# Kernel optimization log

Hardware: AMD Instinct MI355X
Metric: run time of the kernel (lower is better)

## Reference

```python
import jax, jax.numpy as jnp
import numpy as np

B, L, D, E = 16, 1024, 512, 8
DFF = 4 * D
N_VIEWS, N_BUCKETS = 4, 16


def setup_inputs() -> dict:
    key = jax.random.key(0)
    ks = jax.random.split(key, 9)
    s_in = 1.0 / np.sqrt(D)
    s_hid = 1.0 / np.sqrt(DFF)
    return {
        "x": jax.random.normal(ks[0], (B, L, D), dtype=jnp.float32),
        "view_ids": jax.random.randint(ks[1], (B,), 0, N_VIEWS),
        "visit_ids": jax.random.randint(ks[2], (B,), 0, N_BUCKETS),
        "router_view": jax.random.normal(ks[3], (N_VIEWS, E), dtype=jnp.float32),
        "router_visit": jax.random.normal(ks[4], (N_BUCKETS, E), dtype=jnp.float32),
        "W1": jax.random.uniform(ks[5], (E, D, DFF), jnp.float32, -s_in, s_in),
        "b1": jax.random.uniform(ks[6], (E, DFF), jnp.float32, -s_in, s_in),
        "W2": jax.random.uniform(ks[7], (E, DFF, D), jnp.float32, -s_hid, s_hid),
        "b2": jax.random.uniform(ks[8], (E, D), jnp.float32, -s_hid, s_hid),
    }


def reference(x, view_ids, visit_ids, router_view, router_visit, W1, b1, W2, b2):
    # Router: per-sample logits over experts, (B, E)
    logits = router_view[view_ids] + router_visit[visit_ids]
    top1 = jnp.argmax(logits, axis=-1)  # (B,)

    # Train-mode balance loss: load = mean softmax prob per expert, entropy-style term
    probs = jax.nn.softmax(logits, axis=-1)
    load = probs.mean(axis=0)  # (E,)
    balance_loss = -jnp.sum(load * jnp.log(load))

    # Per-sample expert FFN: gather each sample's expert weights (dense grouped GEMM
    # equivalent of the original masked gather->FFN->scatter loop).
    w1 = W1[top1]                      # (B, D, DFF)
    w2 = W2[top1]                      # (B, DFF, D)
    h = jax.nn.relu(jnp.einsum("bld,bdf->blf", x, w1) + b1[top1][:, None, :])
    out = jnp.einsum("blf,bfd->bld", h, w2) + b2[top1][:, None, :]
    return out, balance_loss
```

## Files before the change

### kernel.cpp

```cpp
#include <hip/hip_runtime.h>
#include <stdint.h>

#define B_SZ 16
#define L_SZ 1024
#define D_SZ 512
#define E_SZ 8
#define DFF_SZ 2048

typedef short bf16x8 __attribute__((ext_vector_type(8)));
typedef float f32x4 __attribute__((ext_vector_type(4)));

__device__ __forceinline__ unsigned short f2bf(float f) {
  unsigned int u = __float_as_uint(f);
  u += 0x7fffu + ((u >> 16) & 1u);
  return (unsigned short)(u >> 16);
}

__device__ __forceinline__ void async_cp16(void* lds, const void* g) {
  __builtin_amdgcn_global_load_lds(
      (const __attribute__((address_space(1))) void*)g,
      (__attribute__((address_space(3))) void*)lds, 16, 0, 0);
}

__global__ void router_kernel(const int* __restrict__ view_ids,
                              const int* __restrict__ visit_ids,
                              const float* __restrict__ rview,
                              const float* __restrict__ rvisit,
                              int* __restrict__ top1,
                              float* __restrict__ loss_out) {
  __shared__ float probs[B_SZ][E_SZ];
  const int t = threadIdx.x;
  if (t < B_SZ) {
    const int vi = view_ids[t];
    const int si = visit_ids[t];
    float lg[E_SZ];
#pragma unroll
    for (int e = 0; e < E_SZ; ++e)
      lg[e] = rview[vi * E_SZ + e] + rvisit[si * E_SZ + e];
    int am = 0;
    float bm = lg[0];
#pragma unroll
    for (int e = 1; e < E_SZ; ++e)
      if (lg[e] > bm) { bm = lg[e]; am = e; }
    top1[t] = am;
    float s = 0.f;
#pragma unroll
    for (int e = 0; e < E_SZ; ++e) {
      const float p = expf(lg[e] - bm);
      probs[t][e] = p;
      s += p;
    }
    const float inv = 1.f / s;
#pragma unroll
    for (int e = 0; e < E_SZ; ++e) probs[t][e] *= inv;
  }
  __syncthreads();
  if (t == 0) {
    float loss = 0.f;
#pragma unroll
    for (int e = 0; e < E_SZ; ++e) {
      float ld = 0.f;
      for (int b = 0; b < B_SZ; ++b) ld += probs[b][e];
      ld *= (1.0f / B_SZ);
      loss -= ld * logf(ld);
    }
    *loss_out = loss;
  }
}

__global__ void cast_x_kernel(const float* __restrict__ x,
                              unsigned short* __restrict__ xb) {
  const int i = blockIdx.x * 256 + threadIdx.x;
  const float4 v = reinterpret_cast<const float4*>(x)[i];
  ushort4 o;
  o.x = f2bf(v.x); o.y = f2bf(v.y); o.z = f2bf(v.z); o.w = f2bf(v.w);
  reinterpret_cast<ushort4*>(xb)[i] = o;
}

__global__ void transpose_cast_kernel(const float* __restrict__ src,
                                      unsigned short* __restrict__ dst,
                                      int K, int N) {
  __shared__ float tile[64][65];
  const int e = blockIdx.z;
  const int n0 = blockIdx.x * 64;
  const int k0 = blockIdx.y * 64;
  const int t = threadIdx.x;
  const int c = t & 63;
  const int r4 = t >> 6;
  const float* s = src + ((size_t)e * K + k0) * N + n0;
#pragma unroll
  for (int it = 0; it < 16; ++it) {
    const int k = it * 4 + r4;
    tile[k][c] = s[(size_t)k * N + c];
  }
  __syncthreads();
  unsigned short* d = dst + ((size_t)e * N + n0) * K + k0;
#pragma unroll
  for (int it = 0; it < 16; ++it) {
    const int n = it * 4 + r4;
    d[(size_t)n * K + c] = f2bf(tile[c][n]);
  }
}

template <int BN, int WN2, int NTILES, bool RELU, bool OUT_BF16>
__global__ __launch_bounds__(512, 2) void gemm8_kernel(
    const unsigned short* __restrict__ A,
    const unsigned short* __restrict__ BT,
    const float* __restrict__ bias,
    const int* __restrict__ top1,
    void* __restrict__ Out,
    int N, int K) {
  constexpr int HB = BN / 2;
  constexpr int WM2 = 8 / WN2;
  constexpr int RPA = 128 / WM2;
  constexpr int RPB = HB / WN2;
  constexpr int MF = RPA / 16;
  constexpr int NF = RPB / 16;
  constexpr int LB = HB / 64;
  constexpr int ABUF = 2 * 128 * 64;
  constexpr int BBUF = 2 * HB * 64;
  constexpr int BUFSZ = ABUF + BBUF;

  __shared__ __align__(16) unsigned short sm[2 * BUFSZ];

  const int t = threadIdx.x;
  const int lane = t & 63;
  const int wid = t >> 6;
  const int wm2 = wid / WN2;
  const int wn2 = wid % WN2;
  const int lr = lane & 15, lg = lane >> 4;

  const int nwg = gridDim.x;
  const int bid = blockIdx.x;
  const int wg = (bid & 7) * (nwg >> 3) + (bid >> 3);
  const int mt = wg / NTILES;
  const int nt = wg % NTILES;
  const int n0 = nt * BN;
  const int bz = mt >> 2;
  const int e = top1[bz];

  const size_t Kb = (size_t)K * 2;
  const int srow = t >> 3;
  const int sgr = (t & 7) ^ (srow & 7);
  const char* aRow = (const char*)A + ((size_t)mt * 256 + srow) * Kb + sgr * 16;
  const char* bRow =
      (const char*)BT + ((size_t)e * N + n0 + srow) * Kb + sgr * 16;

  auto stageA = [&](int buf, int half, int kt) {
    char* dst = (char*)sm + (size_t)(buf * BUFSZ + half * (128 * 64)) * 2 + t * 16;
    const char* s = aRow + (size_t)(half * 128) * Kb + (size_t)kt * 128;
    async_cp16(dst, s);
    async_cp16(dst + 8192, s + 64 * Kb);
  };
  auto stageB = [&](int buf, int half, int kt) {
    char* dst =
        (char*)sm + (size_t)(buf * BUFSZ + ABUF + half * (HB * 64)) * 2 + t * 16;
    const char* s = bRow + (size_t)(half * HB) * Kb + (size_t)kt * 128;
    async_cp16(dst, s);
    if constexpr (LB == 2) async_cp16(dst + 8192, s + 64 * Kb);
  };

  f32x4 acc[2][2][MF][NF] = {};
  const int nk = K >> 6;

  stageA(0, 0, 0); stageB(0, 0, 0); stageA(0, 1, 0); stageB(0, 1, 0);
  stageA(1, 0, 1); stageB(1, 0, 1);
  if constexpr (LB == 2) asm volatile("s_waitcnt vmcnt(4)" ::: "memory");
  else                   asm volatile("s_waitcnt vmcnt(3)" ::: "memory");
  __builtin_amdgcn_s_barrier();
  asm volatile("" ::: "memory");

#define PHASE(QM, QN, STAGE_STMT, TAIL_STMT)                                   \
  {                                                                            \
    const char* ab =                                                           \
        (const char*)sm + (size_t)(bi * BUFSZ + (QM) * (128 * 64)) * 2;        \
    const char* bbp =                                                          \
        (const char*)sm + (size_t)(bi * BUFSZ + ABUF + (QN) * (HB * 64)) * 2;  \
    bf16x8 af[MF][2], bg[NF][2];                                               \
    _Pragma("unroll") for (int mf = 0; mf < MF; ++mf) {                        \
      const int row = wm2 * RPA + mf * 16 + lr;                                \
      _Pragma("unroll") for (int ks = 0; ks < 2; ++ks)                         \
          af[mf][ks] = *(const bf16x8*)(ab + row * 128 +                       \
                                        (((ks * 4 + lg) ^ (lr & 7)) << 4));    \
    }                                                                          \
    _Pragma("unroll") for (int nf = 0; nf < NF; ++nf) {                        \
      const int row = wn2 * RPB + nf * 16 + lr;                                \
      _Pragma("unroll") for (int ks = 0; ks < 2; ++ks)                         \
          bg[nf][ks] = *(const bf16x8*)(bbp + row * 128 +                      \
                                        (((ks * 4 + lg) ^ (lr & 7)) << 4));    \
    }                                                                          \
    STAGE_STMT                                                                 \
    __builtin_amdgcn_s_barrier();                                              \
    asm volatile("" ::: "memory");                                             \
    __builtin_amdgcn_s_setprio(1);                                             \
    _Pragma("unroll") for (int ks = 0; ks < 2; ++ks)                           \
        _Pragma("unroll") for (int mf = 0; mf < MF; ++mf)                      \
            _Pragma("unroll") for (int nf = 0; nf < NF; ++nf)                  \
                acc[QM][QN][mf][nf] = __builtin_amdgcn_mfma_f32_16x16x32_bf16( \
                    af[mf][ks], bg[nf][ks], acc[QM][QN][mf][nf], 0, 0, 0);     \
    __builtin_amdgcn_s_setprio(0);                                             \
    TAIL_STMT                                                                  \
    __builtin_amdgcn_s_barrier();                                              \
    asm volatile("" ::: "memory");                                             \
  }

  for (int kt = 0; kt < nk; ++kt) {
    const int bi = kt & 1;
    PHASE(0, 0, { if (kt + 1 < nk) stageA(bi ^ 1, 1, kt + 1); }, {})
    PHASE(0, 1, { if (kt + 1 < nk) stageB(bi ^ 1, 1, kt + 1); }, {})
    PHASE(1, 0, { if (kt + 2 < nk) stageA(bi, 0, kt + 2); }, {})
    PHASE(1, 1, { if (kt + 2 < nk) stageB(bi, 0, kt + 2); },
          {
            if (kt + 2 < nk) {
              if constexpr (LB == 2)
                asm volatile("s_waitcnt vmcnt(4)" ::: "memory");
              else
                asm volatile("s_waitcnt vmcnt(3)" ::: "memory");
            } else {
              asm volatile("s_waitcnt vmcnt(0)" ::: "memory");
            }
          })
  }
#undef PHASE

  const size_t mrow0 = (size_t)mt * 256;
  const float* bp = bias + (size_t)e * N + n0;
  unsigned short* ho = (unsigned short*)Out;
  float* fo = (float*)Out;
#pragma unroll
  for (int qm = 0; qm < 2; ++qm)
#pragma unroll
    for (int mf = 0; mf < MF; ++mf) {
      const int row0 = qm * 128 + wm2 * RPA + mf * 16 + lg * 4;
#pragma unroll
      for (int qn = 0; qn < 2; ++qn)
#pragma unroll
        for (int nf = 0; nf < NF; ++nf) {
          const int col = qn * HB + wn2 * RPB + nf * 16 + lr;
          const float bv = bp[col];
#pragma unroll
          for (int r = 0; r < 4; ++r) {
            float v = acc[qm][qn][mf][nf][r] + bv;
            if (RELU) v = fmaxf(v, 0.f);
            const size_t o = (mrow0 + row0 + r) * (size_t)N + n0 + col;
            if (OUT_BF16) ho[o] = f2bf(v);
            else fo[o] = v;
          }
        }
    }
}

extern "C" void kernel_launch(void* const* d_in, const int* in_sizes, int n_in,
                              void* d_out, int out_size, void* d_ws,
                              size_t ws_size, hipStream_t stream) {
  const float* x = (const float*)d_in[0];
  const int* view_ids = (const int*)d_in[1];
  const int* visit_ids = (const int*)d_in[2];
  const float* rview = (const float*)d_in[3];
  const float* rvisit = (const float*)d_in[4];
  const float* W1 = (const float*)d_in[5];
  const float* b1 = (const float*)d_in[6];
  const float* W2 = (const float*)d_in[7];
  const float* b2 = (const float*)d_in[8];
  float* out = (float*)d_out;

  char* ws = (char*)d_ws;
  int* top1 = (int*)ws;
  unsigned short* x_bf = (unsigned short*)(ws + 256);
  unsigned short* w1t = (unsigned short*)(ws + 256 + 16777216L);
  unsigned short* w2t = (unsigned short*)(ws + 256 + 2 * 16777216L);
  unsigned short* h_bf = (unsigned short*)(ws + 256 + 3 * 16777216L);

  router_kernel<<<1, 64, 0, stream>>>(view_ids, visit_ids, rview, rvisit, top1,
                                      out + (size_t)B_SZ * L_SZ * D_SZ);
  cast_x_kernel<<<8192, 256, 0, stream>>>(x, x_bf);
  transpose_cast_kernel<<<dim3(DFF_SZ / 64, D_SZ / 64, E_SZ), 256, 0, stream>>>(
      W1, w1t, D_SZ, DFF_SZ);
  transpose_cast_kernel<<<dim3(D_SZ / 64, DFF_SZ / 64, E_SZ), 256, 0, stream>>>(
      W2, w2t, DFF_SZ, D_SZ);

  gemm8_kernel<256, 4, 8, true, true><<<512, 512, 0, stream>>>(
      x_bf, w1t, b1, top1, (void*)h_bf, DFF_SZ, D_SZ);
  gemm8_kernel<128, 2, 4, false, false><<<256, 512, 0, stream>>>(
      h_bf, w2t, b2, top1, (void*)out, D_SZ, DFF_SZ);
}
```

Before: 255.1 us.

## Reuse A/B LDS fragments across quadrant phases and vectorize weight transpose-cast

The GEMM main loop now keeps A fragments in registers across the two N-quadrants and keeps both B fragment halves, so each K-step reads A and B from LDS once per half instead of once per quadrant. This cuts LDS read traffic and ds_read instructions in the MFMA loop, at the cost of more live VGPRs (two B fragment sets), which may pressure the 512-thread, 2-waves launch bound. The transpose-cast kernel also switches to float4 global loads and ushort4 stores to reduce memory instruction count.

Measured after the change: 245.3 us. -3.9%, faster.

```diff
diff --git a/kernel.cpp b/kernel.cpp
--- a/kernel.cpp
+++ b/kernel.cpp
@@ -85,20 +85,31 @@
   const int n0 = blockIdx.x * 64;
   const int k0 = blockIdx.y * 64;
   const int t = threadIdx.x;
-  const int c = t & 63;
-  const int r4 = t >> 6;
-  const float* s = src + ((size_t)e * K + k0) * N + n0;
-#pragma unroll
-  for (int it = 0; it < 16; ++it) {
-    const int k = it * 4 + r4;
-    tile[k][c] = s[(size_t)k * N + c];
+  {
+    const int c4 = (t & 15) * 4;
+    const int r = t >> 4;
+    const float* s = src + ((size_t)e * K + k0) * N + n0;
+#pragma unroll
+    for (int i = 0; i < 4; ++i) {
+      const int k = r + i * 16;
+      const float4 v = *(const float4*)(s + (size_t)k * N + c4);
+      tile[k][c4] = v.x; tile[k][c4 + 1] = v.y;
+      tile[k][c4 + 2] = v.z; tile[k][c4 + 3] = v.w;
+    }
   }
   __syncthreads();
-  unsigned short* d = dst + ((size_t)e * N + n0) * K + k0;
-#pragma unroll
-  for (int it = 0; it < 16; ++it) {
-    const int n = it * 4 + r4;
-    d[(size_t)n * K + c] = f2bf(tile[c][n]);
+  {
+    const int k4 = (t & 15) * 4;
+    const int r = t >> 4;
+    unsigned short* d = dst + ((size_t)e * N + n0) * K + k0;
+#pragma unroll
+    for (int i = 0; i < 4; ++i) {
+      const int n = r + i * 16;
+      ushort4 o;
+      o.x = f2bf(tile[k4 + 0][n]); o.y = f2bf(tile[k4 + 1][n]);
+      o.z = f2bf(tile[k4 + 2][n]); o.w = f2bf(tile[k4 + 3][n]);
+      *(ushort4*)(d + (size_t)n * K + k4) = o;
+    }
   }
 }
 
@@ -147,81 +158,98 @@
       (const char*)BT + ((size_t)e * N + n0 + srow) * Kb + sgr * 16;
 
   auto stageA = [&](int buf, int half, int kt) {
-    char* dst = (char*)sm + (size_t)(buf * BUFSZ + half * (128 * 64)) * 2 + t * 16;
+    char* dst =
+        (char*)sm + (size_t)(buf * BUFSZ + half * (128 * 64)) * 2 + t * 16;
     const char* s = aRow + (size_t)(half * 128) * Kb + (size_t)kt * 128;
     async_cp16(dst, s);
     async_cp16(dst + 8192, s + 64 * Kb);
   };
   auto stageB = [&](int buf, int half, int kt) {
-    char* dst =
-        (char*)sm + (size_t)(buf * BUFSZ + ABUF + half * (HB * 64)) * 2 + t * 16;
+    char* dst = (char*)sm + (size_t)(buf * BUFSZ + ABUF + half * (HB * 64)) * 2 +
+                t * 16;
     const char* s = bRow + (size_t)(half * HB) * Kb + (size_t)kt * 128;
     async_cp16(dst, s);
     if constexpr (LB == 2) async_cp16(dst + 8192, s + 64 * Kb);
   };
 
   f32x4 acc[2][2][MF][NF] = {};
+  bf16x8 af[MF][2];
+  bf16x8 bg[2][NF][2];
   const int nk = K >> 6;
+
+#define READ_A(HALF)                                                          \
+  {                                                                           \
+    const char* ap = bufBase + (size_t)(HALF) * (128 * 64 * 2);               \
+    _Pragma("unroll") for (int mf = 0; mf < MF; ++mf) {                       \
+      const int row = wm2 * RPA + mf * 16 + lr;                               \
+      _Pragma("unroll") for (int ks = 0; ks < 2; ++ks)                        \
+          af[mf][ks] = *(const bf16x8*)(ap + row * 128 +                      \
+                                        (((ks * 4 + lg) ^ (lr & 7)) << 4));   \
+    }                                                                         \
+  }
+#define READ_B(Q, HALF)                                                       \
+  {                                                                           \
+    const char* bp =                                                          \
+        bufBase + (size_t)ABUF * 2 + (size_t)(HALF) * (HB * 64 * 2);          \
+    _Pragma("unroll") for (int nf = 0; nf < NF; ++nf) {                       \
+      const int row = wn2 * RPB + nf * 16 + lr;                               \
+      _Pragma("unroll") for (int ks = 0; ks < 2; ++ks)                        \
+          bg[Q][nf][ks] = *(const bf16x8*)(bp + row * 128 +                   \
+                                           (((ks * 4 + lg) ^ (lr & 7)) << 4)); \
+    }                                                                         \
+  }
+#define MMA(QM, QN)                                                           \
+  __builtin_amdgcn_s_setprio(1);                                              \
+  _Pragma("unroll") for (int ks = 0; ks < 2; ++ks)                            \
+      _Pragma("unroll") for (int mf = 0; mf < MF; ++mf)                       \
+          _Pragma("unroll") for (int nf = 0; nf < NF; ++nf)                   \
+              acc[QM][QN][mf][nf] = __builtin_amdgcn_mfma_f32_16x16x32_bf16(  \
+                  af[mf][ks], bg[QN][nf][ks], acc[QM][QN][mf][nf], 0, 0, 0);  \
+  __builtin_amdgcn_s_setprio(0);
+#define BAR                                                                   \
+  __builtin_amdgcn_s_barrier();                                               \
+  asm volatile("" ::: "memory");
 
   stageA(0, 0, 0); stageB(0, 0, 0); stageA(0, 1, 0); stageB(0, 1, 0);
   stageA(1, 0, 1); stageB(1, 0, 1);
   if constexpr (LB == 2) asm volatile("s_waitcnt vmcnt(4)" ::: "memory");
   else                   asm volatile("s_waitcnt vmcnt(3)" ::: "memory");
-  __builtin_amdgcn_s_barrier();
-  asm volatile("" ::: "memory");
-
-#define PHASE(QM, QN, STAGE_STMT, TAIL_STMT)                                   \
-  {                                                                            \
-    const char* ab =                                                           \
-        (const char*)sm + (size_t)(bi * BUFSZ + (QM) * (128 * 64)) * 2;        \
-    const char* bbp =                                                          \
-        (const char*)sm + (size_t)(bi * BUFSZ + ABUF + (QN) * (HB * 64)) * 2;  \
-    bf16x8 af[MF][2], bg[NF][2];                                               \
-    _Pragma("unroll") for (int mf = 0; mf < MF; ++mf) {                        \
-      const int row = wm2 * RPA + mf * 16 + lr;                                \
-      _Pragma("unroll") for (int ks = 0; ks < 2; ++ks)                         \
-          af[mf][ks] = *(const bf16x8*)(ab + row * 128 +                       \
-                                        (((ks * 4 + lg) ^ (lr & 7)) << 4));    \
-    }                                                                          \
-    _Pragma("unroll") for (int nf = 0; nf < NF; ++nf) {                        \
-      const int row = wn2 * RPB + nf * 16 + lr;                                \
-      _Pragma("unroll") for (int ks = 0; ks < 2; ++ks)                         \
-          bg[nf][ks] = *(const bf16x8*)(bbp + row * 128 +                      \
-                                        (((ks * 4 + lg) ^ (lr & 7)) << 4));    \
-    }                                                                          \
-    STAGE_STMT                                                                 \
-    __builtin_amdgcn_s_barrier();                                              \
-    asm volatile("" ::: "memory");                                             \
-    __builtin_amdgcn_s_setprio(1);                                             \
-    _Pragma("unroll") for (int ks = 0; ks < 2; ++ks)                           \
-        _Pragma("unroll") for (int mf = 0; mf < MF; ++mf)                      \
-            _Pragma("unroll") for (int nf = 0; nf < NF; ++nf)                  \
-                acc[QM][QN][mf][nf] = __builtin_amdgcn_mfma_f32_16x16x32_bf16( \
-                    af[mf][ks], bg[nf][ks], acc[QM][QN][mf][nf], 0, 0, 0);     \
-    __builtin_amdgcn_s_setprio(0);                                             \
-    TAIL_STMT                                                                  \
-    __builtin_amdgcn_s_barrier();                                              \
-    asm volatile("" ::: "memory");                                             \
-  }
+  BAR;
 
   for (int kt = 0; kt < nk; ++kt) {
     const int bi = kt & 1;
-    PHASE(0, 0, { if (kt + 1 < nk) stageA(bi ^ 1, 1, kt + 1); }, {})
-    PHASE(0, 1, { if (kt + 1 < nk) stageB(bi ^ 1, 1, kt + 1); }, {})
-    PHASE(1, 0, { if (kt + 2 < nk) stageA(bi, 0, kt + 2); }, {})
-    PHASE(1, 1, { if (kt + 2 < nk) stageB(bi, 0, kt + 2); },
-          {
-            if (kt + 2 < nk) {
-              if constexpr (LB == 2)
-                asm volatile("s_waitcnt vmcnt(4)" ::: "memory");
-              else
-                asm volatile("s_waitcnt vmcnt(3)" ::: "memory");
-            } else {
-              asm volatile("s_waitcnt vmcnt(0)" ::: "memory");
-            }
-          })
-  }
-#undef PHASE
+    const char* bufBase = (const char*)sm + (size_t)bi * BUFSZ * 2;
+    READ_A(0);
+    READ_B(0, 0);
+    if (kt + 1 < nk) stageA(bi ^ 1, 1, kt + 1);
+    BAR;
+    MMA(0, 0);
+    BAR;
+    READ_B(1, 1);
+    if (kt + 1 < nk) stageB(bi ^ 1, 1, kt + 1);
+    BAR;
+    MMA(0, 1);
+    BAR;
+    READ_A(1);
+    if (kt + 2 < nk) stageA(bi, 0, kt + 2);
+    BAR;
+    MMA(1, 0);
+    BAR;
+    if (kt + 2 < nk) stageB(bi, 0, kt + 2);
+    BAR;
+    MMA(1, 1);
+    if (kt + 2 < nk) {
+      if constexpr (LB == 2) asm volatile("s_waitcnt vmcnt(4)" ::: "memory");
+      else                   asm volatile("s_waitcnt vmcnt(3)" ::: "memory");
+    } else {
+      asm volatile("s_waitcnt vmcnt(0)" ::: "memory");
+    }
+    BAR;
+  }
+#undef READ_A
+#undef READ_B
+#undef MMA
+#undef BAR
 
   const size_t mrow0 = (size_t)mt * 256;
   const float* bp = bias + (size_t)e * N + n0;
```
